# Optimization experiments

Hardware: AMD Instinct MI355X
Metric: run time of the kernel (lower is better)

Reference implementation:

```python
import jax, jax.numpy as jnp
import numpy as np

H, W = 256, 832
B = 2
SEARCH_W, SEARCH_H = 7, 3
SPARSITY_RAD = 2
SENSE_RANGE = 10
PIX_W = 20.0          # pixel_distance_weight
ALPHA_W = 0.7         # alpha_distance_weight
MULLINE_W = 15.0      # pixel_mulline_distance_weight
ALPHA_PAD = 0.6       # alpha_padding
INF = 1e9


def _sorted_offsets(span_x, span_y):
    xs, ys = np.meshgrid(span_x, span_y)
    xs = xs.flatten(); ys = ys.flatten()
    order = np.argsort(xs ** 2 + ys ** 2, kind='stable')
    return xs[order].astype(np.int32), ys[order].astype(np.int32)


def setup_inputs() -> dict:
    key = jax.random.key(0)
    k1, k2 = jax.random.split(key)
    src = (jax.random.uniform(k1, (B, 1, H, W)) < 0.02).astype(jnp.float32)
    dst = (jax.random.uniform(k2, (B, 1, H, W)) < 0.02).astype(jnp.float32)
    xx, yy = _sorted_offsets(np.arange(-SEARCH_W, SEARCH_W + 1), np.arange(-SEARCH_H, SEARCH_H + 1))
    sxs, sys_ = np.meshgrid(np.arange(-SPARSITY_RAD, SPARSITY_RAD + 1), np.arange(-SPARSITY_RAD, SPARSITY_RAD + 1))
    sxx = sxs.flatten().astype(np.int32); syy = sys_.flatten().astype(np.int32)
    cxx, cyy = _sorted_offsets(np.arange(-SENSE_RANGE, SENSE_RANGE + 1), np.arange(-SENSE_RANGE, SENSE_RANGE + 1))
    return {"binMapsrc": src, "binMapdst": dst,
            "xx": jnp.asarray(xx), "yy": jnp.asarray(yy),
            "sxx": jnp.asarray(sxx), "syy": jnp.asarray(syy),
            "cxx": jnp.asarray(cxx), "cyy": jnp.asarray(cyy)}


def _orientation(m):
    # local edge orientation from a 3x3 box-blurred map
    b = sum(jnp.roll(jnp.roll(m, di, 0), dj, 1) for di in (-1, 0, 1) for dj in (-1, 0, 1))
    gy, gx = jnp.gradient(b)
    return jnp.arctan2(gy, gx)


def _morph_single(src, dst, xx, yy, sxx, syy, cxx, cyy):
    gy, gx = jnp.meshgrid(jnp.arange(H, dtype=jnp.int32), jnp.arange(W, dtype=jnp.int32), indexing='ij')

    def gather(offy, offx, arr, fill):
        ii = gy[None] + offy[:, None, None]          # [K,H,W]
        jj = gx[None] + offx[:, None, None]
        inb = (ii >= 0) & (ii < H) & (jj >= 0) & (jj < W)
        vals = arr[jnp.clip(ii, 0, H - 1), jnp.clip(jj, 0, W - 1)]
        return jnp.where(inb, vals, fill)

    src_e = src > 0.5
    # --- sparsify source edge points: keep min-linear-index edge in each sparsity window ---
    lin = jnp.where(src_e, (gy * W + gx).astype(jnp.float32), INF)
    keep = src_e & (lin == gather(syy, sxx, lin, INF).min(0))
    # --- windowed correspondence search with distance + orientation scoring ---
    theta_s = _orientation(src)
    theta_d = _orientation(dst)
    hit = gather(yy, xx, dst, 0.0) > 0.5             # [K,H,W]
    ang = 1.0 - jnp.cos(theta_s[None] - gather(yy, xx, theta_d, 0.0))
    dist = jnp.sqrt((xx * xx + yy * yy).astype(jnp.float32))
    score = jnp.where(hit, PIX_W * dist[:, None, None] + MULLINE_W * ALPHA_W * ang, INF)
    kbest = jnp.argmin(score, axis=0)                # [H,W]
    active = keep & (score.min(0) < 0.5 * INF)
    dispx = jnp.where(active, xx[kbest].astype(jnp.float32), 0.0)
    dispy = jnp.where(active, yy[kbest].astype(jnp.float32), 0.0)
    # --- diffuse sparse displacements over the sense window (scan keeps memory small) ---
    R = SENSE_RANGE
    pad = lambda a: jnp.pad(a, ((R, R), (R, R)))
    pdx, pdy, pm = pad(dispx), pad(dispy), pad(active.astype(jnp.float32))
    wk = jnp.exp(-jnp.sqrt((cxx * cxx + cyy * cyy).astype(jnp.float32)) / (0.5 * R))

    def body(carry, inp):
        nx, ny, den = carry
        dy_, dx_, w = inp
        sl = lambda a: jax.lax.dynamic_slice(a, (R + dy_, R + dx_), (H, W))
        return (nx + w * sl(pdx), ny + w * sl(pdy), den + w * sl(pm)), None

    zeros = jnp.zeros((H, W), jnp.float32)
    (nx, ny, den), _ = jax.lax.scan(body, (zeros, zeros, zeros), (cyy, cxx, wk))
    mdx = ALPHA_PAD * nx / (den + 1e-6)
    mdy = ALPHA_PAD * ny / (den + 1e-6)
    morphedx = gx.astype(jnp.float32) + mdx
    morphedy = gy.astype(jnp.float32) + mdy
    return jnp.stack([morphedx, morphedy], 0)        # [2,H,W]


def reference(binMapsrc, binMapdst, xx, yy, sxx, syy, cxx, cyy):
    f = lambda s, d: _morph_single(s, d, xx, yy, sxx, syy, cxx, cyy)
    return jax.vmap(f)(binMapsrc[:, 0], binMapdst[:, 0])  # [B,2,H,W]
```

## Files before the change

### kernel.cpp

```cpp
#include <hip/hip_runtime.h>
#include <math.h>

#define BB 2
#define HH 256
#define WW 832
#define HWIMG (HH * WW)

#define TX2 52
#define TY2 16
#define SEG 64
#define ECAP 192

__device__ inline float theta_at(const float* __restrict__ m, int i, int j) {
    int ri[5], cj[5];
#pragma unroll
    for (int t = 0; t < 5; ++t) {
        int r = i + t - 2; r = (r < 0) ? r + HH : (r >= HH ? r - HH : r);
        int c = j + t - 2; c = (c < 0) ? c + WW : (c >= WW ? c - WW : c);
        ri[t] = r * WW; cj[t] = c;
    }
    float S[5][5];
#pragma unroll
    for (int a = 0; a < 5; ++a)
#pragma unroll
        for (int c = 0; c < 5; ++c)
            S[a][c] = m[ri[a] + cj[c]];
    float ct[5], cm[5], cb[5];
#pragma unroll
    for (int c = 0; c < 5; ++c) {
        ct[c] = S[0][c] + S[1][c] + S[2][c];
        cm[c] = S[1][c] + S[2][c] + S[3][c];
        cb[c] = S[2][c] + S[3][c] + S[4][c];
    }
    float Bm = ct[1] + ct[2] + ct[3];
    float Bp = cb[1] + cb[2] + cb[3];
    float Bl = cm[0] + cm[1] + cm[2];
    float Br = cm[2] + cm[3] + cm[4];
    float Bc = cm[1] + cm[2] + cm[3];
    float gy = (i == 0) ? (Bp - Bc) : (i == HH - 1) ? (Bc - Bm) : 0.5f * (Bp - Bm);
    float gx = (j == 0) ? (Br - Bc) : (j == WW - 1) ? (Bc - Bl) : 0.5f * (Br - Bl);
    return atan2f(gy, gx);
}

__global__ void prep_search_kernel(const float* __restrict__ src, const float* __restrict__ dst,
                                   const int* __restrict__ xx, const int* __restrict__ yy, int K,
                                   int* __restrict__ cnt, int* __restrict__ seg) {
    __shared__ int kox[128], koy[128];
    __shared__ float kd[128];
    __shared__ int recs[SEG];
    __shared__ float tss[SEG];
    __shared__ int outv[SEG];
    __shared__ int nkeep;

    int tid = threadIdx.x;
    if (tid == 0) nkeep = 0;
    for (int t = tid; t < K; t += 256) {
        int ox = xx[t], oy = yy[t];
        kox[t] = ox; koy[t] = oy;
        kd[t] = 20.0f * sqrtf((float)(ox * ox + oy * oy));
    }
    __syncthreads();

    int txi = blockIdx.x, tyi = blockIdx.y, b = blockIdx.z;
    int gi = tyi * 16 + (tid >> 4);
    int gj = txi * 16 + (tid & 15);
    const float* sb = src + b * HWIMG;
    const float* db = dst + b * HWIMG;

    if (sb[gi * WW + gj] > 0.5f) {
        float m = 0.f;
#pragma unroll
        for (int p = 0; p < 12; ++p) {
            int di = (p < 5) ? -2 : (p < 10 ? -1 : 0);
            int dj = (p < 5) ? (p - 2) : (p < 10 ? (p - 7) : (p - 12));
            int ii = gi + di, jj = gj + dj;
            bool inb = (ii >= 0) && (jj >= 0) && (jj < WW);
            float v = sb[inb ? (ii * WW + jj) : 0];
            m = fmaxf(m, inb ? v : 0.f);
        }
        if (m <= 0.5f) {
            float ts = theta_at(sb, gi, gj);
            int pos = atomicAdd(&nkeep, 1);
            if (pos < SEG) { recs[pos] = gj | (gi << 10); tss[pos] = ts; }
        }
    }
    __syncthreads();

    int nk = (nkeep < SEG) ? nkeep : SEG;
    int lane = tid & 63;
    int wv = tid >> 6;
    for (int w = wv; w < nk; w += 4) {
        int rec = recs[w];
        int kj = rec & 1023;
        int ki = rec >> 10;
        float ts = tss[w];

        float best = 1e9f;
        int bk = 1 << 20;
#pragma unroll
        for (int rr = 0; rr < 2; ++rr) {
            int k = lane + rr * 64;
            if (k < K) {
                int pi = ki + koy[k], pj = kj + kox[k];
                if (pi >= 0 && pi < HH && pj >= 0 && pj < WW && db[pi * WW + pj] > 0.5f) {
                    float td = theta_at(db, pi, pj);
                    float sc = kd[k] + 10.5f * (1.0f - cosf(ts - td));
                    if (sc < best || (sc == best && k < bk)) { best = sc; bk = k; }
                }
            }
        }
#pragma unroll
        for (int off = 32; off >= 1; off >>= 1) {
            float ob = __shfl_down(best, off, 64);
            int ok = __shfl_down(bk, off, 64);
            if (ob < best || (ob == best && ok < bk)) { best = ob; bk = ok; }
        }
        if (lane == 0)
            outv[w] = (best < 5e8f)
                ? (rec | (b << 18) | ((kox[bk] + 7) << 19) | ((koy[bk] + 3) << 23))
                : -1;
    }
    __syncthreads();

    int tile = (b * TY2 + tyi) * TX2 + txi;
    if (tid < nk) seg[tile * SEG + tid] = outv[tid];
    if (tid == 0) cnt[tile] = nk;
}

__global__ void diffuse_kernel(const int* __restrict__ cnt, const int* __restrict__ seg,
                               float* __restrict__ out) {
    __shared__ float wt[441];
    __shared__ float4 ent[ECAP];
    __shared__ int ncnt[9];
    __shared__ int ne;

    int tid = threadIdx.x;
    if (tid == 0) ne = 0;
    for (int t = tid; t < 441; t += 256) {
        int dy = t / 21 - 10;
        int dx = t % 21 - 10;
        wt[t] = expf(-sqrtf((float)(dx * dx + dy * dy)) / 5.0f);
    }
    int txi = blockIdx.x, tyi = blockIdx.y, b = blockIdx.z;
    if (tid < 9) {
        int nty = tyi + tid / 3 - 1;
        int ntx = txi + tid % 3 - 1;
        ncnt[tid] = (nty >= 0 && nty < TY2 && ntx >= 0 && ntx < TX2)
                        ? cnt[(b * TY2 + nty) * TX2 + ntx] : 0;
    }
    __syncthreads();

    for (int t = tid; t < 9 * SEG; t += 256) {
        int q = t / SEG, slot = t % SEG;
        if (slot < ncnt[q]) {
            int nty = tyi + q / 3 - 1;
            int ntx = txi + q % 3 - 1;
            int v = seg[((b * TY2 + nty) * TX2 + ntx) * SEG + slot];
            if (v != -1) {
                int pos = atomicAdd(&ne, 1);
                if (pos < ECAP)
                    ent[pos] = make_float4((float)(v & 1023), (float)((v >> 10) & 255),
                                           (float)(((v >> 19) & 15) - 7),
                                           (float)(((v >> 23) & 7) - 3));
            }
        }
    }
    __syncthreads();

    int nn = (ne < ECAP) ? ne : ECAP;
    int gj = txi * 16 + (tid & 15);
    int gi = tyi * 16 + (tid >> 4);
    float nx = 0.f, ny = 0.f, de = 0.f;
    for (int c = 0; c < nn; ++c) {
        float4 E = ent[c];
        int dj = (int)E.x - gj;
        int di = (int)E.y - gi;
        if (dj >= -10 && dj <= 10 && di >= -10 && di <= 10) {
            float w = wt[(di + 10) * 21 + dj + 10];
            de += w; nx += w * E.z; ny += w * E.w;
        }
    }
    float inv = 0.6f / (de + 1e-6f);
    int obase = b * 2 * HWIMG;
    out[obase + gi * WW + gj] = (float)gj + nx * inv;
    out[obase + HWIMG + gi * WW + gj] = (float)gi + ny * inv;
}

extern "C" void kernel_launch(void* const* d_in, const int* in_sizes, int n_in,
                              void* d_out, int out_size, void* d_ws, size_t ws_size,
                              hipStream_t stream) {
    const float* src = (const float*)d_in[0];
    const float* dst = (const float*)d_in[1];
    const int* xx = (const int*)d_in[2];
    const int* yy = (const int*)d_in[3];
    int K = in_sizes[2];

    int* cnt = (int*)d_ws;
    int* seg = cnt + BB * TY2 * TX2;
    float* out = (float*)d_out;

    dim3 grid(TX2, TY2, BB);
    prep_search_kernel<<<grid, dim3(256), 0, stream>>>(src, dst, xx, yy, K, cnt, seg);
    diffuse_kernel<<<grid, dim3(256), 0, stream>>>(cnt, seg, out);
}
```

Before: 91.78 us.

## Fuse sparsify/search and diffusion into one kernel with halo recomputation

```diff
diff --git a/kernel.cpp b/kernel.cpp
--- a/kernel.cpp
+++ b/kernel.cpp
@@ -8,8 +8,7 @@
 
 #define TX2 52
 #define TY2 16
-#define SEG 64
-#define ECAP 192
+#define ECAP 256
 
 __device__ inline float theta_at(const float* __restrict__ m, int i, int j) {
     int ri[5], cj[5];
@@ -42,14 +41,13 @@
     return atan2f(gy, gx);
 }
 
-__global__ void prep_search_kernel(const float* __restrict__ src, const float* __restrict__ dst,
-                                   const int* __restrict__ xx, const int* __restrict__ yy, int K,
-                                   int* __restrict__ cnt, int* __restrict__ seg) {
+__global__ void bnmorph_kernel(const float* __restrict__ src, const float* __restrict__ dst,
+                               const int* __restrict__ xx, const int* __restrict__ yy, int K,
+                               float* __restrict__ out) {
     __shared__ int kox[128], koy[128];
     __shared__ float kd[128];
-    __shared__ int recs[SEG];
-    __shared__ float tss[SEG];
-    __shared__ int outv[SEG];
+    __shared__ float wt[441];
+    __shared__ float4 ent[ECAP];
     __shared__ int nkeep;
 
     int tid = threadIdx.x;
@@ -59,131 +57,101 @@
         kox[t] = ox; koy[t] = oy;
         kd[t] = 20.0f * sqrtf((float)(ox * ox + oy * oy));
     }
-    __syncthreads();
-
-    int txi = blockIdx.x, tyi = blockIdx.y, b = blockIdx.z;
-    int gi = tyi * 16 + (tid >> 4);
-    int gj = txi * 16 + (tid & 15);
-    const float* sb = src + b * HWIMG;
-    const float* db = dst + b * HWIMG;
-
-    if (sb[gi * WW + gj] > 0.5f) {
-        float m = 0.f;
-#pragma unroll
-        for (int p = 0; p < 12; ++p) {
-            int di = (p < 5) ? -2 : (p < 10 ? -1 : 0);
-            int dj = (p < 5) ? (p - 2) : (p < 10 ? (p - 7) : (p - 12));
-            int ii = gi + di, jj = gj + dj;
-            bool inb = (ii >= 0) && (jj >= 0) && (jj < WW);
-            float v = sb[inb ? (ii * WW + jj) : 0];
-            m = fmaxf(m, inb ? v : 0.f);
-        }
-        if (m <= 0.5f) {
-            float ts = theta_at(sb, gi, gj);
-            int pos = atomicAdd(&nkeep, 1);
-            if (pos < SEG) { recs[pos] = gj | (gi << 10); tss[pos] = ts; }
-        }
-    }
-    __syncthreads();
-
-    int nk = (nkeep < SEG) ? nkeep : SEG;
-    int lane = tid & 63;
-    int wv = tid >> 6;
-    for (int w = wv; w < nk; w += 4) {
-        int rec = recs[w];
-        int kj = rec & 1023;
-        int ki = rec >> 10;
-        float ts = tss[w];
-
-        float best = 1e9f;
-        int bk = 1 << 20;
-#pragma unroll
-        for (int rr = 0; rr < 2; ++rr) {
-            int k = lane + rr * 64;
-            if (k < K) {
-                int pi = ki + koy[k], pj = kj + kox[k];
-                if (pi >= 0 && pi < HH && pj >= 0 && pj < WW && db[pi * WW + pj] > 0.5f) {
-                    float td = theta_at(db, pi, pj);
-                    float sc = kd[k] + 10.5f * (1.0f - cosf(ts - td));
-                    if (sc < best || (sc == best && k < bk)) { best = sc; bk = k; }
-                }
-            }
-        }
-#pragma unroll
-        for (int off = 32; off >= 1; off >>= 1) {
-            float ob = __shfl_down(best, off, 64);
-            int ok = __shfl_down(bk, off, 64);
-            if (ob < best || (ob == best && ok < bk)) { best = ob; bk = ok; }
-        }
-        if (lane == 0)
-            outv[w] = (best < 5e8f)
-                ? (rec | (b << 18) | ((kox[bk] + 7) << 19) | ((koy[bk] + 3) << 23))
-                : -1;
-    }
-    __syncthreads();
-
-    int tile = (b * TY2 + tyi) * TX2 + txi;
-    if (tid < nk) seg[tile * SEG + tid] = outv[tid];
-    if (tid == 0) cnt[tile] = nk;
-}
-
-__global__ void diffuse_kernel(const int* __restrict__ cnt, const int* __restrict__ seg,
-                               float* __restrict__ out) {
-    __shared__ float wt[441];
-    __shared__ float4 ent[ECAP];
-    __shared__ int ncnt[9];
-    __shared__ int ne;
-
-    int tid = threadIdx.x;
-    if (tid == 0) ne = 0;
     for (int t = tid; t < 441; t += 256) {
         int dy = t / 21 - 10;
         int dx = t % 21 - 10;
         wt[t] = expf(-sqrtf((float)(dx * dx + dy * dy)) / 5.0f);
     }
-    int txi = blockIdx.x, tyi = blockIdx.y, b = blockIdx.z;
-    if (tid < 9) {
-        int nty = tyi + tid / 3 - 1;
-        int ntx = txi + tid % 3 - 1;
-        ncnt[tid] = (nty >= 0 && nty < TY2 && ntx >= 0 && ntx < TX2)
-                        ? cnt[(b * TY2 + nty) * TX2 + ntx] : 0;
-    }
     __syncthreads();
 
-    for (int t = tid; t < 9 * SEG; t += 256) {
-        int q = t / SEG, slot = t % SEG;
-        if (slot < ncnt[q]) {
-            int nty = tyi + q / 3 - 1;
-            int ntx = txi + q % 3 - 1;
-            int v = seg[((b * TY2 + nty) * TX2 + ntx) * SEG + slot];
-            if (v != -1) {
-                int pos = atomicAdd(&ne, 1);
-                if (pos < ECAP)
-                    ent[pos] = make_float4((float)(v & 1023), (float)((v >> 10) & 255),
-                                           (float)(((v >> 19) & 15) - 7),
-                                           (float)(((v >> 23) & 7) - 3));
+    int ti = blockIdx.y * 16, tj = blockIdx.x * 16;
+    int b = blockIdx.z;
+    const float* sb = src + b * HWIMG;
+    const float* db = dst + b * HWIMG;
+
+    for (int t = tid; t < 36 * 36; t += 256) {
+        int gi = ti - 10 + t / 36;
+        int gj = tj - 10 + t % 36;
+        if (gi < 0 || gi >= HH || gj < 0 || gj >= WW) continue;
+        if (sb[gi * WW + gj] > 0.5f) {
+            float m = 0.f;
+#pragma unroll
+            for (int p = 0; p < 12; ++p) {
+                int di = (p < 5) ? -2 : (p < 10 ? -1 : 0);
+                int dj = (p < 5) ? (p - 2) : (p < 10 ? (p - 7) : (p - 12));
+                int ii = gi + di, jj = gj + dj;
+                bool inb = (ii >= 0) && (jj >= 0) && (jj < WW);
+                float v = sb[inb ? (ii * WW + jj) : 0];
+                m = fmaxf(m, inb ? v : 0.f);
+            }
+            if (m <= 0.5f) {
+                float ts = theta_at(sb, gi, gj);
+                int pos = atomicAdd(&nkeep, 1);
+                if (pos < ECAP) ent[pos] = make_float4((float)gj, (float)gi, ts, 0.f);
             }
         }
     }
     __syncthreads();
 
-    int nn = (ne < ECAP) ? ne : ECAP;
-    int gj = txi * 16 + (tid & 15);
-    int gi = tyi * 16 + (tid >> 4);
-    float nx = 0.f, ny = 0.f, de = 0.f;
-    for (int c = 0; c < nn; ++c) {
-        float4 E = ent[c];
-        int dj = (int)E.x - gj;
-        int di = (int)E.y - gi;
-        if (dj >= -10 && dj <= 10 && di >= -10 && di <= 10) {
-            float w = wt[(di + 10) * 21 + dj + 10];
-            de += w; nx += w * E.z; ny += w * E.w;
+    int nk = (nkeep < ECAP) ? nkeep : ECAP;
+    {
+        int lane = tid & 63;
+        int wv = tid >> 6;
+        for (int w = wv; w < nk; w += 4) {
+            float4 E = ent[w];
+            int kj = (int)E.x, ki = (int)E.y;
+            float ts = E.z;
+
+            float best = 1e9f;
+            int bk = 1 << 20;
+#pragma unroll
+            for (int rr = 0; rr < 2; ++rr) {
+                int k = lane + rr * 64;
+                if (k < K) {
+                    int pi = ki + koy[k], pj = kj + kox[k];
+                    if (pi >= 0 && pi < HH && pj >= 0 && pj < WW && db[pi * WW + pj] > 0.5f) {
+                        float td = theta_at(db, pi, pj);
+                        float sc = kd[k] + 10.5f * (1.0f - cosf(ts - td));
+                        if (sc < best || (sc == best && k < bk)) { best = sc; bk = k; }
+                    }
+                }
+            }
+#pragma unroll
+            for (int off = 32; off >= 1; off >>= 1) {
+                float ob = __shfl_down(best, off, 64);
+                int ok = __shfl_down(bk, off, 64);
+                if (ob < best || (ob == best && ok < bk)) { best = ob; bk = ok; }
+            }
+            if (lane == 0) {
+                if (best < 5e8f) {
+                    ent[w].z = (float)kox[bk];
+                    ent[w].w = (float)koy[bk];
+                } else {
+                    ent[w].x = -1e4f;
+                }
+            }
         }
     }
-    float inv = 0.6f / (de + 1e-6f);
-    int obase = b * 2 * HWIMG;
-    out[obase + gi * WW + gj] = (float)gj + nx * inv;
-    out[obase + HWIMG + gi * WW + gj] = (float)gi + ny * inv;
+    __syncthreads();
+
+    {
+        int gj = tj + (tid & 15);
+        int gi = ti + (tid >> 4);
+        float nx = 0.f, ny = 0.f, de = 0.f;
+        for (int c = 0; c < nk; ++c) {
+            float4 E = ent[c];
+            int dj = (int)E.x - gj;
+            int di = (int)E.y - gi;
+            if (dj >= -10 && dj <= 10 && di >= -10 && di <= 10) {
+                float w = wt[(di + 10) * 21 + dj + 10];
+                de += w; nx += w * E.z; ny += w * E.w;
+            }
+        }
+        float inv = 0.6f / (de + 1e-6f);
+        int obase = b * 2 * HWIMG;
+        out[obase + gi * WW + gj] = (float)gj + nx * inv;
+        out[obase + HWIMG + gi * WW + gj] = (float)gi + ny * inv;
+    }
 }
 
 extern "C" void kernel_launch(void* const* d_in, const int* in_sizes, int n_in,
@@ -195,11 +163,6 @@
     const int* yy = (const int*)d_in[3];
     int K = in_sizes[2];
 
-    int* cnt = (int*)d_ws;
-    int* seg = cnt + BB * TY2 * TX2;
-    float* out = (float*)d_out;
-
-    dim3 grid(TX2, TY2, BB);
-    prep_search_kernel<<<grid, dim3(256), 0, stream>>>(src, dst, xx, yy, K, cnt, seg);
-    diffuse_kernel<<<grid, dim3(256), 0, stream>>>(cnt, seg, out);
+    bnmorph_kernel<<<dim3(TX2, TY2, BB), dim3(256), 0, stream>>>(
+        src, dst, xx, yy, K, (float*)d_out);
 }
```

After: 111.6 us. 21.6% more time.
